# Optimization experiments

Measured on AMD Instinct MI355X. Metric: run time of the kernel, lower is better.

The kernel has to match this reference:

```python
import jax, jax.numpy as jnp
import numpy as np

NEG = jnp.float32(-1e9)
N_PRE = 12000   # n_train_pre_nms (module default training=True)
N_POST = 2000   # n_train_post_nms
MIN_SIZE = 16.0
NMS_THRESH = 0.7


def _make_anchors(feat_size=64, stride=16):
    scales = np.array([128.0, 256.0, 512.0])
    ratios = np.array([0.5, 1.0, 2.0])
    ws = (scales[:, None] * np.sqrt(1.0 / ratios)[None, :]).reshape(-1)  # [9]
    hs = (scales[:, None] * np.sqrt(ratios)[None, :]).reshape(-1)        # [9]
    ctr = (np.arange(feat_size) + 0.5) * stride
    cy, cx = np.meshgrid(ctr, ctr, indexing='ij')
    cx = cx.reshape(-1, 1); cy = cy.reshape(-1, 1)                       # [4096,1]
    x1 = cx - 0.5 * ws[None, :]; y1 = cy - 0.5 * hs[None, :]
    x2 = cx + 0.5 * ws[None, :]; y2 = cy + 0.5 * hs[None, :]
    return np.stack([x1, y1, x2, y2], axis=-1).reshape(-1, 4).astype(np.float32)  # [36864,4]


def setup_inputs() -> dict:
    key = jax.random.key(0)
    k1, k2 = jax.random.split(key)
    anchors = jnp.asarray(_make_anchors())[None]            # [1, 36864, 4]
    B, N = 8, anchors.shape[1]
    pred_loc = jax.random.normal(k1, (B, N, 4), jnp.float32) * 0.2
    pred_obj = jax.random.normal(k2, (B, N, 2), jnp.float32)
    return {"img_height": 1024, "img_width": 1024,
            "anchor_boxes": anchors, "pred_loc": pred_loc, "pred_obj": pred_obj}


def _decode(anchors, loc, img_w, img_h):
    # anchors [N,4] (x1,y1,x2,y2), loc [N,4] (dx,dy,dw,dh)
    w = anchors[:, 2] - anchors[:, 0]
    h = anchors[:, 3] - anchors[:, 1]
    cx = anchors[:, 0] + 0.5 * w
    cy = anchors[:, 1] + 0.5 * h
    pcx = loc[:, 0] * w + cx
    pcy = loc[:, 1] * h + cy
    pw = jnp.exp(loc[:, 2]) * w
    ph = jnp.exp(loc[:, 3]) * h
    x1 = jnp.clip(pcx - 0.5 * pw, 0.0, img_w)
    y1 = jnp.clip(pcy - 0.5 * ph, 0.0, img_h)
    x2 = jnp.clip(pcx + 0.5 * pw, 0.0, img_w)
    y2 = jnp.clip(pcy + 0.5 * ph, 0.0, img_h)
    return jnp.stack([x1, y1, x2, y2], axis=-1)  # [N,4]


def _iou_one_vs_all(box, boxes):
    # box [4], boxes [M,4]
    ix1 = jnp.maximum(box[0], boxes[:, 0])
    iy1 = jnp.maximum(box[1], boxes[:, 1])
    ix2 = jnp.minimum(box[2], boxes[:, 2])
    iy2 = jnp.minimum(box[3], boxes[:, 3])
    inter = jnp.maximum(ix2 - ix1, 0.0) * jnp.maximum(iy2 - iy1, 0.0)
    a0 = (box[2] - box[0]) * (box[3] - box[1])
    a1 = (boxes[:, 2] - boxes[:, 0]) * (boxes[:, 3] - boxes[:, 1])
    return inter / jnp.maximum(a0 + a1 - inter, 1e-9)


def _greedy_nms(boxes, scores):
    # boxes [M,4], scores [M] (invalid entries already NEG). Selects the first
    # N_POST boxes kept by greedy IoU suppression (exactly torchvision nms +
    # [:n_post] truncation, since greedy NMS emits in descending-score order).
    def step(s, _):
        i = jnp.argmax(s)
        valid = s[i] > NEG * 0.5
        box = boxes[i]
        suppress = _iou_one_vs_all(box, boxes) > NMS_THRESH  # includes self
        s = jnp.where(suppress, NEG, s)
        return s, (box, valid)
    _, (kept, mask) = jax.lax.scan(step, scores, None, length=N_POST)
    return jnp.where(mask[:, None], kept, 0.0), mask  # [N_POST,4], [N_POST]


def reference(img_height, img_width, anchor_boxes, pred_loc, pred_obj):
    img_h = jnp.float32(img_height)
    img_w = jnp.float32(img_width)
    anchors = anchor_boxes[0]                                    # [N,4]
    scores = jax.nn.softmax(pred_obj, axis=2)[:, :, 1]           # [B,N]
    boxes = jax.vmap(lambda l: _decode(anchors, l, img_w, img_h))(pred_loc)  # [B,N,4]
    # min-size filter -> mask scores instead of dynamic filtering
    valid = jnp.all(boxes[..., 2:] - boxes[..., :2] >= MIN_SIZE, axis=-1)    # [B,N]
    scores = jnp.where(valid, scores, NEG)
    # descending sort + pre-NMS truncation == top_k
    top_s, top_i = jax.lax.top_k(scores, N_PRE)                  # [B,N_PRE]
    top_boxes = jnp.take_along_axis(boxes, top_i[..., None], axis=1)         # [B,N_PRE,4]
    kept_boxes, kept_mask = jax.vmap(_greedy_nms)(top_boxes, top_s)
    return kept_boxes, kept_mask  # [B,N_POST,4] padded, [B,N_POST] validity
```

## Files before the change

### kernel.cpp

```cpp
#include <hip/hip_runtime.h>

typedef unsigned long long u64;
typedef unsigned int u32;

#define B_SZ   8
#define N_ANC  36864
#define N_PRE  12000
#define N_POST 2000
#define SEG    2048
#define NSEG   6
#define MAXC   (SEG * NSEG)
#define NW     (SEG / 64)
#define NDW    (MAXC / 64)
#define NBLK   144

__device__ __forceinline__ float area_of(float4 p) {
  return __fmul_rn(__fsub_rn(p.z, p.x), __fsub_rn(p.w, p.y));
}

__device__ __forceinline__ bool iou_gt_a(float4 p, float4 q, float a0, float a1) {
  float ix1 = fmaxf(p.x, q.x), iy1 = fmaxf(p.y, q.y);
  float ix2 = fminf(p.z, q.z), iy2 = fminf(p.w, q.w);
  float iw = fmaxf(__fsub_rn(ix2, ix1), 0.0f);
  float ih = fmaxf(__fsub_rn(iy2, iy1), 0.0f);
  float inter = __fmul_rn(iw, ih);
  float den = fmaxf(__fsub_rn(__fadd_rn(a0, a1), inter), 1e-9f);
  return (inter / den) > 0.7f;
}

__global__ __launch_bounds__(256) void k_decode(
    const int* __restrict__ imh_p, const int* __restrict__ imw_p,
    const float* __restrict__ anchors, const float* __restrict__ loc,
    const float* __restrict__ obj, float4* __restrict__ boxes,
    u64* __restrict__ keys, u32* __restrict__ hist)
{
  __shared__ u32 lh[2048];
  int t = threadIdx.x;
#pragma unroll
  for (int i = 0; i < 8; ++i) lh[t + i * 256] = 0;
  __syncthreads();

  int n = blockIdx.x * 256 + t;
  int b = blockIdx.y;
  float a0 = anchors[n * 4 + 0], a1 = anchors[n * 4 + 1];
  float a2 = anchors[n * 4 + 2], a3 = anchors[n * 4 + 3];
  size_t off = (size_t)b * N_ANC + n;
  float l0 = loc[off * 4 + 0], l1 = loc[off * 4 + 1];
  float l2 = loc[off * 4 + 2], l3 = loc[off * 4 + 3];

  float w  = __fsub_rn(a2, a0);
  float h  = __fsub_rn(a3, a1);
  float cx = __fadd_rn(a0, __fmul_rn(0.5f, w));
  float cy = __fadd_rn(a1, __fmul_rn(0.5f, h));
  float pcx = __fadd_rn(__fmul_rn(l0, w), cx);
  float pcy = __fadd_rn(__fmul_rn(l1, h), cy);
  float pw  = __fmul_rn(expf(l2), w);
  float ph  = __fmul_rn(expf(l3), h);
  float imw = (float)imw_p[0], imh = (float)imh_p[0];
  float hx = __fmul_rn(0.5f, pw), hy = __fmul_rn(0.5f, ph);
  float x1 = fminf(fmaxf(__fsub_rn(pcx, hx), 0.0f), imw);
  float y1 = fminf(fmaxf(__fsub_rn(pcy, hy), 0.0f), imh);
  float x2 = fminf(fmaxf(__fadd_rn(pcx, hx), 0.0f), imw);
  float y2 = fminf(fmaxf(__fadd_rn(pcy, hy), 0.0f), imh);
  boxes[off] = make_float4(x1, y1, x2, y2);

  bool valid = (__fsub_rn(x2, x1) >= 16.0f) && (__fsub_rn(y2, y1) >= 16.0f);

  float o0 = obj[off * 2 + 0], o1 = obj[off * 2 + 1];
  float m  = fmaxf(o0, o1);
  float e0 = expf(__fsub_rn(o0, m));
  float e1 = expf(__fsub_rn(o1, m));
  float s  = e1 / __fadd_rn(e0, e1);
  float sc = valid ? s : -1e9f;

  u32 u  = __float_as_uint(sc);
  u32 fk = (u & 0x80000000u) ? ~u : (u | 0x80000000u);
  u32 sk = ~fk;
  u64 key = ((u64)sk << 32) | (u32)n;
  keys[off] = key;
  atomicAdd(&lh[(u32)(key >> 53)], 1u);
  __syncthreads();
#pragma unroll
  for (int i = 0; i < 8; ++i) {
    u32 v = lh[t + i * 256];
    if (v) atomicAdd(&hist[b * 2048 + t + i * 256], v);
  }
}

__global__ __launch_bounds__(256) void k_pick1(
    const u32* __restrict__ hist, u32* __restrict__ T1, u32* __restrict__ Base1)
{
  int b = blockIdx.x, t = threadIdx.x;
  const u32* h = hist + b * 2048;
  __shared__ u32 part[256], pre[256];
  u32 loc[8], s = 0;
#pragma unroll
  for (int i = 0; i < 8; ++i) { loc[i] = h[t * 8 + i]; s += loc[i]; }
  part[t] = s;
  __syncthreads();
  if (t == 0) { u32 acc = 0; for (int i = 0; i < 256; ++i) { pre[i] = acc; acc += part[i]; } }
  __syncthreads();
  u32 acc = pre[t];
#pragma unroll
  for (int i = 0; i < 8; ++i) {
    u32 na = acc + loc[i];
    if (acc < N_PRE && na >= N_PRE) { T1[b] = (u32)(t * 8 + i); Base1[b] = acc; }
    acc = na;
  }
}

__global__ __launch_bounds__(256) void k_hist2(
    const u64* __restrict__ keys, const u32* __restrict__ T1,
    u32* __restrict__ hist)
{
  int b = blockIdx.y;
  u32 t1 = T1[b];
  __shared__ u32 lh[2048];
  int t = threadIdx.x;
#pragma unroll
  for (int i = 0; i < 8; ++i) lh[t + i * 256] = 0;
  __syncthreads();
#pragma unroll
  for (int k = 0; k < 4; ++k) {
    int i = blockIdx.x * 1024 + k * 256 + t;
    u64 key = keys[(size_t)b * N_ANC + i];
    if ((u32)(key >> 53) == t1) atomicAdd(&lh[(u32)(key >> 42) & 0x7FFu], 1u);
  }
  __syncthreads();
#pragma unroll
  for (int i = 0; i < 8; ++i) {
    u32 v = lh[t + i * 256];
    if (v) atomicAdd(&hist[b * 2048 + t + i * 256], v);
  }
}

__global__ __launch_bounds__(256) void k_pick2(
    const u32* __restrict__ hist, const u32* __restrict__ T1,
    const u32* __restrict__ Base1, u32* __restrict__ T2)
{
  int b = blockIdx.x, t = threadIdx.x;
  const u32* h = hist + b * 2048;
  __shared__ u32 part[256], pre[256];
  u32 loc[8], s = 0;
#pragma unroll
  for (int i = 0; i < 8; ++i) { loc[i] = h[t * 8 + i]; s += loc[i]; }
  part[t] = s;
  __syncthreads();
  if (t == 0) { u32 acc = Base1[b]; for (int i = 0; i < 256; ++i) { pre[i] = acc; acc += part[i]; } }
  __syncthreads();
  u32 acc = pre[t];
#pragma unroll
  for (int i = 0; i < 8; ++i) {
    u32 na = acc + loc[i];
    if (acc < N_PRE && na >= N_PRE) T2[b] = (T1[b] << 11) | (u32)(t * 8 + i);
    acc = na;
  }
}

__global__ __launch_bounds__(256) void k_count(
    const u64* __restrict__ keys, const u32* __restrict__ T2,
    u32* __restrict__ bcnt)
{
  int b = blockIdx.y;
  int i = blockIdx.x * 256 + threadIdx.x;
  u64 key = keys[(size_t)b * N_ANC + i];
  bool pred = (u32)(key >> 42) <= T2[b];
  u64 bal = __ballot(pred);
  __shared__ u32 wc[4];
  int wv = threadIdx.x >> 6, lane = threadIdx.x & 63;
  if (lane == 0) wc[wv] = (u32)__popcll(bal);
  __syncthreads();
  if (threadIdx.x == 0)
    bcnt[b * NBLK + blockIdx.x] = wc[0] + wc[1] + wc[2] + wc[3];
}

__global__ __launch_bounds__(256) void k_scatter(
    const u64* __restrict__ keys, const u32* __restrict__ T2,
    const u32* __restrict__ bcnt, u64* __restrict__ cand)
{
  int b = blockIdx.y, bx = blockIdx.x;
  int t = threadIdx.x;
  __shared__ u32 cnts[NBLK];
  __shared__ u32 wc[4];
  __shared__ u32 sbase;
  if (t < NBLK) cnts[t] = bcnt[b * NBLK + t];
  u64 key = keys[(size_t)b * N_ANC + bx * 256 + t];
  bool pred = (u32)(key >> 42) <= T2[b];
  u64 bal = __ballot(pred);
  int wv = t >> 6, lane = t & 63;
  if (lane == 0) wc[wv] = (u32)__popcll(bal);
  __syncthreads();
  if (t == 0) { u32 a = 0; for (int i = 0; i < bx; ++i) a += cnts[i]; sbase = a; }
  __syncthreads();
  u32 base = sbase;
  for (int w = 0; w < wv; ++w) base += wc[w];
  u32 rank = (u32)__popcll(bal & ((1ull << lane) - 1ull));
  if (pred) {
    u32 pos = base + rank;
    if (pos < MAXC) cand[(size_t)b * MAXC + pos] = key;
  }
}

#define SIDX(x) ((x) + ((x) >> 5))
__global__ __launch_bounds__(1024) void k_sort_tile(u64* __restrict__ a)
{
  int b = blockIdx.y, base = blockIdx.x * 2048;
  u64* p = a + (size_t)b * MAXC + base;
  __shared__ u64 lds[2048 + 64];
  int t = threadIdx.x;
  lds[SIDX(t)] = p[t];
  lds[SIDX(t + 1024)] = p[t + 1024];
  __syncthreads();
  for (int k = 2; k <= 2048; k <<= 1) {
    for (int j = k >> 1; j > 0; j >>= 1) {
      int i = ((t & ~(j - 1)) << 1) | (t & (j - 1));
      int l = i | j;
      bool asc = ((i & k) == 0);
      u64 x = lds[SIDX(i)], y = lds[SIDX(l)];
      if ((x > y) == asc) { lds[SIDX(i)] = y; lds[SIDX(l)] = x; }
      __syncthreads();
    }
  }
  p[t] = lds[SIDX(t)];
  p[t + 1024] = lds[SIDX(t + 1024)];
}

__global__ __launch_bounds__(256) void k_merge_gather(
    const u64* __restrict__ cand, const float4* __restrict__ boxes,
    float4* __restrict__ gbox, u64* __restrict__ deadm)
{
  int b = blockIdx.y;
  int p = blockIdx.x * 256 + threadIdx.x;
  const u64* cb = cand + (size_t)b * MAXC;
  u64 key = cb[p];
  int r = p >> 11;
  int rank = p & 2047;
#pragma unroll
  for (int s = 0; s < NSEG; ++s) {
    if (s == r) continue;
    const u64* run = cb + (s << 11);
    int lo = 0;
#pragma unroll
    for (int step = 2048; step >= 1; step >>= 1) {
      int np = lo + step;
      if (np <= 2048 && run[np - 1] < key) lo = np;
    }
    rank += lo;
  }
  bool valid = ((u32)(key >> 32) < 0x80000000u) && (rank < N_PRE);
  float4 bx = make_float4(0.f, 0.f, 0.f, 0.f);
  if (valid) bx = boxes[(size_t)b * N_ANC + (u32)key];
  gbox[(size_t)b * MAXC + rank] = bx;
  if (!valid) atomicOr(&deadm[b * NDW + (rank >> 6)], 1ull << (rank & 63));
}

__device__ __forceinline__ void segmask_tile(
    int b, int sg, int tile, const float4* __restrict__ gbox,
    u64* __restrict__ smask, u64* __restrict__ smaskT,
    float4* rbox, float* rarea, u64* diag)
{
  int r = tile, rg = 0;
  while (r >= 32 - rg) { r -= 32 - rg; ++rg; }
  int cw = rg + r;
  const float4* gb = gbox + (size_t)b * MAXC + sg * SEG;
  int t = threadIdx.x;
  if (t < 64) { float4 bx = gb[rg * 64 + t]; rbox[t] = bx; rarea[t] = area_of(bx); }
  __syncthreads();
  int wv = t >> 6, lane = t & 63;
  u64* srow = smask + (size_t)(b * NSEG + sg) * SEG * NW + (size_t)rg * 64 * NW;
  float4 cb4 = gb[cw * 64 + lane];
  float ca = area_of(cb4);
  bool isdiag = (cw == rg);
  for (int rr = wv * 16; rr < wv * 16 + 16; ++rr) {
    bool p = iou_gt_a(rbox[rr], cb4, rarea[rr], ca);
    if (isdiag) p = p && (lane > rr);
    u64 m = __ballot(p);
    if (lane == 0) { srow[(size_t)rr * NW + cw] = m; if (isdiag) diag[rr] = m; }
  }
  if (isdiag) {
    __syncthreads();
    if (t < 64) {
      u64 s = 0;
      for (int q = 0; q < 64; ++q) s |= ((diag[q] >> t) & 1ull) << q;
      smaskT[(size_t)(b * NSEG + sg) * SEG + rg * 64 + t] = s;
    }
  }
}

__global__ __launch_bounds__(256) void k_segmask01(
    const float4* __restrict__ gbox, u64* __restrict__ smask,
    u64* __restrict__ smaskT)
{
  __shared__ float4 rbox[64]; __shared__ float rarea[64]; __shared__ u64 diag[64];
  int b = blockIdx.y;
  int sg = blockIdx.x / 528, tile = blockIdx.x % 528;
  segmask_tile(b, sg, tile, gbox, smask, smaskT, rbox, rarea, diag);
}

__device__ __forceinline__ void cross_work(
    int b, int sg, int bx, const float4* __restrict__ gbox,
    const float4* __restrict__ keptb, const int* __restrict__ meta,
    u64* __restrict__ deadm, float4* kb, float* ka)
{
  int kc = bx >> 3, cbk = bx & 7;
  int nkept = meta[b * 8 + 0];
  int kbase = kc * 256;
  if (kbase >= nkept) return;
  int kcnt = min(256, nkept - kbase);
  int t = threadIdx.x;
  if (t < kcnt) {
    float4 k4 = keptb[(size_t)b * SEG + kbase + t];
    kb[t] = k4; ka[t] = area_of(k4);
  }
  __syncthreads();
  int gi = sg * SEG + cbk * 256 + t;
  float4 my = gbox[(size_t)b * MAXC + gi];
  float ma = area_of(my);
  bool sup = false;
  for (int kk = 0; kk < kcnt; ++kk) {
    if (iou_gt_a(kb[kk], my, ka[kk], ma)) { sup = true; break; }
  }
  u64 bm = __ballot(sup);
  if ((t & 63) == 0 && bm) atomicOr(&deadm[b * NDW + (gi >> 6)], bm);
}

__global__ __launch_bounds__(256) void k_cross(
    const float4* __restrict__ gbox, const float4* __restrict__ keptb,
    const int* __restrict__ meta, u64* __restrict__ deadm, int sg)
{
  int b = blockIdx.y;
  if (meta[b * 8 + 1]) return;
  __shared__ float4 kb[256]; __shared__ float ka[256];
  cross_work(b, sg, blockIdx.x, gbox, keptb, meta, deadm, kb, ka);
}

__global__ __launch_bounds__(256) void k_crossmask(
    const float4* __restrict__ gbox, const float4* __restrict__ keptb,
    const int* __restrict__ meta, u64* __restrict__ deadm,
    u64* __restrict__ smask, u64* __restrict__ smaskT, int sg)
{
  int b = blockIdx.y;
  if (meta[b * 8 + 1]) return;
  __shared__ float4 kb[256]; __shared__ float ka[256]; __shared__ u64 diag[64];
  if (blockIdx.x < 64) {
    cross_work(b, sg, blockIdx.x, gbox, keptb, meta, deadm, kb, ka);
  } else {
    segmask_tile(b, sg, blockIdx.x - 64, gbox, smask, smaskT,
                 kb, ka, diag);
  }
}

__global__ __launch_bounds__(1024) void k_walk(
    const float4* __restrict__ gbox, const u64* __restrict__ smask,
    const u64* __restrict__ smaskT, const u64* __restrict__ deadm,
    int* __restrict__ meta, float4* __restrict__ keptb,
    float* __restrict__ out, int sg)
{
  int b = blockIdx.x;
  if (meta[b * 8 + 1]) return;
  int t = threadIdx.x, wv = t >> 6, lane = t & 63;

  __shared__ u64 rowbuf[2][2048];
  __shared__ u64 stbuf[2][64];
  __shared__ float4 bbox[2][64];
  __shared__ u64 sdead[2];
  __shared__ u32 remv[64];
  __shared__ u32 klist[64];
  __shared__ int s_stop, s_nkept, s_kcnt;

  const u64* smb = smask + (size_t)(b * NSEG + sg) * SEG * NW;
  const u64* stb = smaskT + (size_t)(b * NSEG + sg) * SEG;
  const u64* dmb = deadm + b * NDW + sg * NW;
  const float4* gb = gbox + (size_t)b * MAXC + sg * SEG;
  float4* kbuf = keptb + (size_t)b * SEG;
  float4* ob = (float4*)(out + (size_t)b * N_POST * 4);
  float* om = out + (size_t)B_SZ * N_POST * 4 + (size_t)b * N_POST;

  {
    u64 a = smb[t], c = smb[t + 1024];
    u64 st_ = 0; float4 bb_ = make_float4(0.f, 0.f, 0.f, 0.f);
    if (t < 64) { st_ = stb[t]; bb_ = gb[t]; }
    u64 sd_ = (t == 0) ? dmb[0] : 0;
    rowbuf[0][t] = a;
    rowbuf[0][t + 1024] = c;
    if (t < 64) { stbuf[0][t] = st_; bbox[0][t] = bb_; remv[t] = 0; }
    if (t == 0) { sdead[0] = sd_; s_stop = 0; s_nkept = meta[b * 8 + 0]; }
  }
  int p0 = t - 64, p1 = p0 + 960, p2 = p0 + 1920;
  u64 ra = 0, rc = 0, re = 0, rst = 0, rsd = 0;
  float4 rbb = make_float4(0.f, 0.f, 0.f, 0.f);
  if (wv > 0) {
    const u64* src = smb + 2048;
    ra = src[p0];
    rc = src[p1];
    if (p0 < 128) re = src[p2];
    if (p0 < 64) { rst = stb[64 + p0]; rbb = gb[64 + p0]; }
    if (t == 64) rsd = dmb[1];
  }
  __syncthreads();

  for (int g = 0; g < NW; ++g) {
    int cb = g & 1, nb = cb ^ 1;
    if (wv > 0) {
      if (g < NW - 1) {
        rowbuf[nb][p0] = ra;
        rowbuf[nb][p1] = rc;
        if (p0 < 128) rowbuf[nb][p2] = re;
        if (p0 < 64) { stbuf[nb][p0] = rst; bbox[nb][p0] = rbb; }
        if (t == 64) sdead[nb] = rsd;
      }
      if (g < NW - 2) {
        const u64* src = smb + (size_t)(g + 2) * 2048;
        ra = src[p0];
        rc = src[p1];
        if (p0 < 128) re = src[p2];
        if (p0 < 64) { rst = stb[(g + 2) * 64 + p0]; rbb = gb[(g + 2) * 64 + p0]; }
        if (t == 64) rsd = dmb[g + 2];
      }
    } else {
      int l = lane;
      u64 S = stbuf[cb][l];
      u64 remg = ((u64)remv[2 * g + 1] << 32) | remv[2 * g];
      u64 avail = ~(remg | sdead[cb]);
      u64 km = 0;
      while (avail) {
        bool al = (avail >> l) & 1;
        u64 newk = __ballot(al && (S & avail) == 0ull);
        u64 nd   = __ballot(al && (S & newk) != 0ull);
        km |= newk;
        avail &= ~(newk | nd);
      }
      int nk0 = s_nkept;
      int rem = N_POST - nk0;
      int kc = __popcll(km);
      bool stop = (kc >= rem);
      int rank = __popcll(km & ((1ull << l) - 1ull));
      if (((km >> l) & 1) && rank < rem) {
        float4 bx = bbox[cb][l];
        kbuf[nk0 + rank] = bx;
        ob[nk0 + rank] = bx;
        om[nk0 + rank] = 1.0f;
        klist[rank] = (u32)l;
      }
      if (l == 0) {
        int eff = stop ? rem : kc;
        s_kcnt = eff;
        s_nkept = nk0 + eff;
        if (stop) s_stop = 1;
      }
    }
    __syncthreads();
    if (s_stop) break;
    if (g < NW - 1) {
      int kcnt = s_kcnt;
      if (kcnt) {
        u32* rb32 = (u32*)rowbuf[cb];
        for (int i = t; i < kcnt * 64; i += 1024) {
          int kk = i >> 6, w = i & 63;
          if ((w >> 1) > g) {
            u32 v = rb32[klist[kk] * 64 + w];
            if (v) atomicOr(&remv[w], v);
          }
        }
      }
    }
    __syncthreads();
  }
  int nk = s_nkept;
  bool fin = s_stop || (sg == NSEG - 1);
  if (t == 0) { meta[b * 8 + 0] = nk; if (fin) meta[b * 8 + 1] = 1; }
  if (fin) {
    float4 zero = make_float4(0.f, 0.f, 0.f, 0.f);
    for (int i = nk + t; i < N_POST; i += 1024) { ob[i] = zero; om[i] = 0.0f; }
  }
}

extern "C" void kernel_launch(void* const* d_in, const int* in_sizes, int n_in,
                              void* d_out, int out_size, void* d_ws, size_t ws_size,
                              hipStream_t stream)
{
  const int*   imh     = (const int*)d_in[0];
  const int*   imw     = (const int*)d_in[1];
  const float* anchors = (const float*)d_in[2];
  const float* loc     = (const float*)d_in[3];
  const float* obj     = (const float*)d_in[4];
  float* out = (float*)d_out;

  char* ws = (char*)d_ws;
  size_t off = 0;
  float4* boxes = (float4*)(ws + off); off += (size_t)B_SZ * N_ANC * 16;
  u64*    keys  = (u64*)   (ws + off); off += (size_t)B_SZ * N_ANC * 8;
  u64*    cand  = (u64*)   (ws + off); off += (size_t)B_SZ * MAXC * 8;
  float4* gbox  = (float4*)(ws + off); off += (size_t)B_SZ * MAXC * 16;
  float4* keptb = (float4*)(ws + off); off += (size_t)B_SZ * SEG * 16;
  off = (off + 255) & ~(size_t)255;
  char*   zr    = ws + off;
  u32*    hist1 = (u32*)(zr);
  u32*    hist2 = (u32*)(zr + 65536);
  u32*    T1    = (u32*)(zr + 131072);
  u32*    Base1 = (u32*)(zr + 131072 + 32);
  u32*    T2    = (u32*)(zr + 131072 + 64);
  int*    meta  = (int*)(zr + 131072 + 128);
  u64*    deadm = (u64*)(zr + 131072 + 128 + 256);
  u32*    bcnt  = (u32*)(zr + 131072 + 128 + 256 + (size_t)B_SZ * NDW * 8);
  size_t  zr_sz = 131072 + 128 + 256 + (size_t)B_SZ * NDW * 8
                + (size_t)B_SZ * NBLK * 4;
  off += (zr_sz + 255) & ~(size_t)255;
  u64*    smask  = (u64*)(ws + off); off += (size_t)B_SZ * NSEG * SEG * NW * 8;
  u64*    smaskT = (u64*)(ws + off); off += (size_t)B_SZ * NSEG * SEG * 8;

  hipMemsetAsync(zr, 0, zr_sz, stream);
  hipMemsetAsync(cand, 0xFF, (size_t)B_SZ * MAXC * 8, stream);

  k_decode<<<dim3(NBLK, B_SZ), 256, 0, stream>>>(imh, imw, anchors, loc, obj,
                                                 boxes, keys, hist1);
  k_pick1<<<B_SZ, 256, 0, stream>>>(hist1, T1, Base1);
  k_hist2<<<dim3(36, B_SZ), 256, 0, stream>>>(keys, T1, hist2);
  k_pick2<<<B_SZ, 256, 0, stream>>>(hist2, T1, Base1, T2);

  k_count<<<dim3(NBLK, B_SZ), 256, 0, stream>>>(keys, T2, bcnt);
  k_scatter<<<dim3(NBLK, B_SZ), 256, 0, stream>>>(keys, T2, bcnt, cand);

  k_sort_tile<<<dim3(NSEG, B_SZ), 1024, 0, stream>>>(cand);
  k_merge_gather<<<dim3(MAXC / 256, B_SZ), 256, 0, stream>>>(cand, boxes, gbox, deadm);

  k_segmask01<<<dim3(1056, B_SZ), 256, 0, stream>>>(gbox, smask, smaskT);

  k_walk<<<B_SZ, 1024, 0, stream>>>(gbox, smask, smaskT, deadm, meta, keptb, out, 0);
  k_cross<<<dim3(64, B_SZ), 256, 0, stream>>>(gbox, keptb, meta, deadm, 1);
  k_walk<<<B_SZ, 1024, 0, stream>>>(gbox, smask, smaskT, deadm, meta, keptb, out, 1);
  for (int sg = 2; sg < NSEG; ++sg) {
    k_crossmask<<<dim3(592, B_SZ), 256, 0, stream>>>(gbox, keptb, meta, deadm,
                                                     smask, smaskT, sg);
    k_walk<<<B_SZ, 1024, 0, stream>>>(gbox, smask, smaskT, deadm, meta, keptb, out, sg);
  }
}
```

Measured before the change: 216.1 us.

## Overlap next segment's suppression-mask build with the serial NMS walk

The intra-segment IoU mask for segment sg+1 is now computed in the same launch as the serial greedy walk over segment sg: block 0 runs the walk and the other 528 blocks (1024 threads, 16 waves each) build the next segment's mask tiles. The cross-segment suppression kernel is split back out, and the walk's barriers use an explicit lgkmcnt wait plus s_barrier. The aim is to hide mask-building time behind the latency-bound single-block walk. In exchange every walk launch carries many extra blocks that compete with the walk block for the GPU, and mask tiles now run with 4 rows per wave instead of 16.

```diff
diff --git a/kernel.cpp b/kernel.cpp
--- a/kernel.cpp
+++ b/kernel.cpp
@@ -26,6 +26,13 @@
   float inter = __fmul_rn(iw, ih);
   float den = fmaxf(__fsub_rn(__fadd_rn(a0, a1), inter), 1e-9f);
   return (inter / den) > 0.7f;
+}
+
+__device__ __forceinline__ void block_sync_lgkm() {
+  __builtin_amdgcn_sched_barrier(0);
+  asm volatile("s_waitcnt lgkmcnt(0)" ::: "memory");
+  __builtin_amdgcn_s_barrier();
+  __builtin_amdgcn_sched_barrier(0);
 }
 
 __global__ __launch_bounds__(256) void k_decode(
@@ -254,11 +261,14 @@
   if (!valid) atomicOr(&deadm[b * NDW + (rank >> 6)], 1ull << (rank & 63));
 }
 
-__device__ __forceinline__ void segmask_tile(
+template <int NWAVES>
+__device__ __forceinline__ void segmask_tile_body(
     int b, int sg, int tile, const float4* __restrict__ gbox,
-    u64* __restrict__ smask, u64* __restrict__ smaskT,
-    float4* rbox, float* rarea, u64* diag)
-{
+    u64* smask, u64* smaskT)
+{
+  __shared__ float4 rbox[64];
+  __shared__ float rarea[64];
+  __shared__ u64 diag[64];
   int r = tile, rg = 0;
   while (r >= 32 - rg) { r -= 32 - rg; ++rg; }
   int cw = rg + r;
@@ -267,11 +277,12 @@
   if (t < 64) { float4 bx = gb[rg * 64 + t]; rbox[t] = bx; rarea[t] = area_of(bx); }
   __syncthreads();
   int wv = t >> 6, lane = t & 63;
+  const int RPW = 64 / NWAVES;
   u64* srow = smask + (size_t)(b * NSEG + sg) * SEG * NW + (size_t)rg * 64 * NW;
   float4 cb4 = gb[cw * 64 + lane];
   float ca = area_of(cb4);
   bool isdiag = (cw == rg);
-  for (int rr = wv * 16; rr < wv * 16 + 16; ++rr) {
+  for (int rr = wv * RPW; rr < wv * RPW + RPW; ++rr) {
     bool p = iou_gt_a(rbox[rr], cb4, rarea[rr], ca);
     if (isdiag) p = p && (lane > rr);
     u64 m = __ballot(p);
@@ -287,22 +298,21 @@
   }
 }
 
-__global__ __launch_bounds__(256) void k_segmask01(
+__global__ __launch_bounds__(256) void k_segmask0(
     const float4* __restrict__ gbox, u64* __restrict__ smask,
     u64* __restrict__ smaskT)
 {
-  __shared__ float4 rbox[64]; __shared__ float rarea[64]; __shared__ u64 diag[64];
+  segmask_tile_body<4>(blockIdx.y, 0, blockIdx.x, gbox, smask, smaskT);
+}
+
+__global__ __launch_bounds__(256) void k_cross(
+    const float4* __restrict__ gbox, const float4* __restrict__ keptb,
+    const int* __restrict__ meta, u64* __restrict__ deadm, int sg)
+{
   int b = blockIdx.y;
-  int sg = blockIdx.x / 528, tile = blockIdx.x % 528;
-  segmask_tile(b, sg, tile, gbox, smask, smaskT, rbox, rarea, diag);
-}
-
-__device__ __forceinline__ void cross_work(
-    int b, int sg, int bx, const float4* __restrict__ gbox,
-    const float4* __restrict__ keptb, const int* __restrict__ meta,
-    u64* __restrict__ deadm, float4* kb, float* ka)
-{
-  int kc = bx >> 3, cbk = bx & 7;
+  if (meta[b * 8 + 1]) return;
+  __shared__ float4 kb[256]; __shared__ float ka[256];
+  int kc = blockIdx.x >> 3, cbk = blockIdx.x & 7;
   int nkept = meta[b * 8 + 0];
   int kbase = kc * 256;
   if (kbase >= nkept) return;
@@ -324,40 +334,12 @@
   if ((t & 63) == 0 && bm) atomicOr(&deadm[b * NDW + (gi >> 6)], bm);
 }
 
-__global__ __launch_bounds__(256) void k_cross(
-    const float4* __restrict__ gbox, const float4* __restrict__ keptb,
-    const int* __restrict__ meta, u64* __restrict__ deadm, int sg)
-{
-  int b = blockIdx.y;
-  if (meta[b * 8 + 1]) return;
-  __shared__ float4 kb[256]; __shared__ float ka[256];
-  cross_work(b, sg, blockIdx.x, gbox, keptb, meta, deadm, kb, ka);
-}
-
-__global__ __launch_bounds__(256) void k_crossmask(
-    const float4* __restrict__ gbox, const float4* __restrict__ keptb,
-    const int* __restrict__ meta, u64* __restrict__ deadm,
-    u64* __restrict__ smask, u64* __restrict__ smaskT, int sg)
-{
-  int b = blockIdx.y;
-  if (meta[b * 8 + 1]) return;
-  __shared__ float4 kb[256]; __shared__ float ka[256]; __shared__ u64 diag[64];
-  if (blockIdx.x < 64) {
-    cross_work(b, sg, blockIdx.x, gbox, keptb, meta, deadm, kb, ka);
-  } else {
-    segmask_tile(b, sg, blockIdx.x - 64, gbox, smask, smaskT,
-                 kb, ka, diag);
-  }
-}
-
-__global__ __launch_bounds__(1024) void k_walk(
-    const float4* __restrict__ gbox, const u64* __restrict__ smask,
-    const u64* __restrict__ smaskT, const u64* __restrict__ deadm,
+__device__ void walk_body(
+    int b, int sg, const float4* __restrict__ gbox, const u64* smask,
+    const u64* smaskT, const u64* __restrict__ deadm,
     int* __restrict__ meta, float4* __restrict__ keptb,
-    float* __restrict__ out, int sg)
-{
-  int b = blockIdx.x;
-  if (meta[b * 8 + 1]) return;
+    float* __restrict__ out)
+{
   int t = threadIdx.x, wv = t >> 6, lane = t & 63;
 
   __shared__ u64 rowbuf[2][2048];
@@ -397,7 +379,7 @@
     if (p0 < 64) { rst = stb[64 + p0]; rbb = gb[64 + p0]; }
     if (t == 64) rsd = dmb[1];
   }
-  __syncthreads();
+  block_sync_lgkm();
 
   for (int g = 0; g < NW; ++g) {
     int cb = g & 1, nb = cb ^ 1;
@@ -449,7 +431,7 @@
         if (stop) s_stop = 1;
       }
     }
-    __syncthreads();
+    block_sync_lgkm();
     if (s_stop) break;
     if (g < NW - 1) {
       int kcnt = s_kcnt;
@@ -464,7 +446,7 @@
         }
       }
     }
-    __syncthreads();
+    block_sync_lgkm();
   }
   int nk = s_nkept;
   bool fin = s_stop || (sg == NSEG - 1);
@@ -472,6 +454,22 @@
   if (fin) {
     float4 zero = make_float4(0.f, 0.f, 0.f, 0.f);
     for (int i = nk + t; i < N_POST; i += 1024) { ob[i] = zero; om[i] = 0.0f; }
+  }
+}
+
+__global__ __launch_bounds__(1024) void k_walkmask(
+    const float4* __restrict__ gbox, u64* smask, u64* smaskT,
+    const u64* __restrict__ deadm, int* __restrict__ meta,
+    float4* __restrict__ keptb, float* __restrict__ out, int sg, int msg)
+{
+  int b = blockIdx.y;
+  if (blockIdx.x == 0) {
+    if (meta[b * 8 + 1]) return;
+    walk_body(b, sg, gbox, smask, smaskT, deadm, meta, keptb, out);
+  } else {
+    if (msg < 0 || msg >= NSEG) return;
+    if (meta[b * 8 + 1]) return;
+    segmask_tile_body<16>(b, msg, blockIdx.x - 1, gbox, smask, smaskT);
   }
 }
 
@@ -524,14 +522,15 @@
   k_sort_tile<<<dim3(NSEG, B_SZ), 1024, 0, stream>>>(cand);
   k_merge_gather<<<dim3(MAXC / 256, B_SZ), 256, 0, stream>>>(cand, boxes, gbox, deadm);
 
-  k_segmask01<<<dim3(1056, B_SZ), 256, 0, stream>>>(gbox, smask, smaskT);
-
-  k_walk<<<B_SZ, 1024, 0, stream>>>(gbox, smask, smaskT, deadm, meta, keptb, out, 0);
-  k_cross<<<dim3(64, B_SZ), 256, 0, stream>>>(gbox, keptb, meta, deadm, 1);
-  k_walk<<<B_SZ, 1024, 0, stream>>>(gbox, smask, smaskT, deadm, meta, keptb, out, 1);
-  for (int sg = 2; sg < NSEG; ++sg) {
-    k_crossmask<<<dim3(592, B_SZ), 256, 0, stream>>>(gbox, keptb, meta, deadm,
-                                                     smask, smaskT, sg);
-    k_walk<<<B_SZ, 1024, 0, stream>>>(gbox, smask, smaskT, deadm, meta, keptb, out, sg);
-  }
-}
+  k_segmask0<<<dim3(528, B_SZ), 256, 0, stream>>>(gbox, smask, smaskT);
+
+  k_walkmask<<<dim3(529, B_SZ), 1024, 0, stream>>>(gbox, smask, smaskT, deadm,
+                                                   meta, keptb, out, 0, 1);
+  for (int sg = 1; sg < NSEG; ++sg) {
+    k_cross<<<dim3(64, B_SZ), 256, 0, stream>>>(gbox, keptb, meta, deadm, sg);
+    int msg = (sg + 1 < NSEG) ? sg + 1 : -1;
+    int gx = (msg >= 0) ? 529 : 1;
+    k_walkmask<<<dim3(gx, B_SZ), 1024, 0, stream>>>(gbox, smask, smaskT, deadm,
+                                                    meta, keptb, out, sg, msg);
+  }
+}
```

Measured after the change: 240.4 us. +11.3%, slower.
